# Optimization experiments

Hardware: AMD Instinct MI355X
Metric: run time of the kernel (lower is better)

## Reference

```python
import jax, jax.numpy as jnp
import numpy as np

ALPHA = 0.01  # alpha = input_scale * weight_scale (dequant scale)
BETA = 1.0    # bias scale, fixed to 1.0 in forward


def setup_inputs() -> dict:
    key = jax.random.key(0)
    k1, k2, k3 = jax.random.split(key, 3)
    # int8 values carried in int32 containers (schema has no int8 dtype)
    x = jax.random.randint(k1, (2, 2048, 4096), -127, 128, dtype=jnp.int32)
    weight = jax.random.randint(k2, (11008, 4096), -127, 128, dtype=jnp.int32)
    bias = jax.random.normal(k3, (1, 11008), dtype=jnp.float32)
    return {"x": x, "weight": weight, "bias": bias}


def reference(x, weight, bias):
    # x: [..., K] int8 activations, weight: [N, K] int8, bias: [1, N] fp32
    x_shape = x.shape
    x2 = x.reshape(-1, x_shape[-1]).astype(jnp.int8)   # [M, K]
    w8 = weight.astype(jnp.int8)                        # [N, K]
    acc = jnp.einsum('mk,nk->mn', x2, w8, preferred_element_type=jnp.int32)
    # fused dequant scale + fp32 bias add
    y = ALPHA * acc.astype(jnp.float32) + BETA * bias   # [M, N]
    return y.reshape(*x_shape[:-1], -1)
```

## Files before the change

kernel.cpp:

```cpp
#include <hip/hip_runtime.h>


#define M_DIM 4096
#define N_DIM 11008
#define K_DIM 4096
#define BM 256
#define BN 256
#define BK 128
#define NT (K_DIM / BK)
#define ALPHA 0.01f

typedef __attribute__((ext_vector_type(4))) int i32x4;

static __device__ __forceinline__ int pack4(int4 v) {
    return (v.x & 0xff) | ((v.y & 0xff) << 8) |
           ((v.z & 0xff) << 16) | ((unsigned)(v.w & 0xff) << 24);
}

__global__ __launch_bounds__(256) void pack_i8_kernel(
    const int4* __restrict__ x, int4* __restrict__ xout, int n16x,
    const int4* __restrict__ w, int4* __restrict__ wout, int n16_total)
{
    int i = blockIdx.x * blockDim.x + threadIdx.x;
    if (i >= n16_total) return;
    const int4* src;
    int4* dst;
    int idx;
    if (i < n16x) { src = x; dst = xout; idx = i; }
    else          { src = w; dst = wout; idx = i - n16x; }
    const int4* p = src + (size_t)4 * idx;
    int4 a = p[0], b = p[1], c = p[2], d = p[3];
    int4 r;
    r.x = pack4(a); r.y = pack4(b); r.z = pack4(c); r.w = pack4(d);
    dst[idx] = r;
}

#define GA0 (s_ + 8 * (s_ >> 3))
#define GA1 (8 + s_ + 8 * (s_ >> 3))

#define STAGE(dstArr, srcB, T, GEXPR)                                          \
    _Pragma("unroll") for (int u_ = 0; u_ < 2; u_++) {                         \
        const int s_ = u_ * 8 + wave;                                          \
        const int G_ = (GEXPR);                                                \
        __builtin_amdgcn_global_load_lds(                                      \
            (const __attribute__((address_space(1))) void*)(                   \
                (srcB) + (size_t)(G_ * 8 + (lane >> 3)) * K_DIM +              \
                (size_t)(T) * BK + sch16),                                     \
            (__attribute__((address_space(3))) void*)((dstArr) + G_ * 1024 +   \
                                                      lane * 16),              \
            16, 0, 0);                                                         \
    }

#define READ_A(Arr, dst, IB)                                                   \
    _Pragma("unroll") for (int i_ = 0; i_ < 4; i_++)                           \
        _Pragma("unroll") for (int k_ = 0; k_ < 2; k_++)                       \
            dst[i_][k_] = *(const i32x4*)((Arr) + aoff[k_] + ((IB) + i_) * 2048);

#define BLOAD01(dst, IMM)                                                      \
    _Pragma("unroll") for (int j_ = 0; j_ < 2; j_++)                           \
        _Pragma("unroll") for (int k_ = 0; k_ < 2; k_++)                       \
            dst[j_][k_] = *(const i32x4*)(bptr[j_] + (IMM) + k_ * 64);
#define BLOAD23(dst, IMM)                                                      \
    _Pragma("unroll") for (int j_ = 0; j_ < 2; j_++)                           \
        _Pragma("unroll") for (int k_ = 0; k_ < 2; k_++)                       \
            dst[j_][k_] = *(const i32x4*)(bptr[2 + j_] + (IMM) + k_ * 64);

#define MFMA_G(af, bf, IB, JB)                                                 \
    __builtin_amdgcn_s_setprio(1);                                             \
    _Pragma("unroll") for (int k_ = 0; k_ < 2; k_++)                           \
        _Pragma("unroll") for (int i_ = 0; i_ < 4; i_++)                       \
            _Pragma("unroll") for (int j_ = 0; j_ < 2; j_++)                   \
                acc[(IB) + i_][(JB) + j_] =                                    \
                    __builtin_amdgcn_mfma_i32_16x16x64_i8(                     \
                        af[i_][k_], bf[j_][k_],                                \
                        acc[(IB) + i_][(JB) + j_], 0, 0, 0);                   \
    __builtin_amdgcn_s_setprio(0);

#define VMCNT_(N) asm volatile("s_waitcnt vmcnt(" #N ")" ::: "memory")
#define VMCNT(N) VMCNT_(N)
#define BAR() __builtin_amdgcn_s_barrier()
#define SCHEDB() __builtin_amdgcn_sched_barrier(0)

#define TILE(CA, NA, B01c, B01n, T, KOFF, STG, V2, V4)                         \
    {                                                                          \
        READ_A(CA, ra, 0);                                             \
        if (STG) { STAGE(NA, Abase, (T) + 1, GA0); }                           \
        MFMA_G(ra, B01c, 0, 0);                                  \
        MFMA_G(ra, rb23, 0, 2);                                  \
        if (STG) { BLOAD01(B01n, (KOFF) + 128);                                \
                   STAGE(NA, Abase, (T) + 1, GA1); }                           \
        VMCNT(V2);                                                             \
        SCHEDB();                                                              \
        BAR();                                                    \
        READ_A(CA, ra, 4);                                             \
        MFMA_G(ra, rb23, 4, 2);                                  \
        if (STG) { BLOAD23(rb23, (KOFF) + 128); }                              \
        MFMA_G(ra, B01c, 4, 0);                                  \
        VMCNT(V4);                                                             \
        SCHEDB();                                                              \
        BAR();                                                    \
    }

__global__ __launch_bounds__(512, 1) void gemm_i8_kernel(
    const char* __restrict__ A,
    const char* __restrict__ B,
    const float* __restrict__ bias,
    float* __restrict__ C)
{
    __shared__ __attribute__((aligned(16))) char As0[BM * BK];
    __shared__ __attribute__((aligned(16))) char As1[BM * BK];

    const int tid   = threadIdx.x;
    const int lane  = tid & 63;
    const int wave  = tid >> 6;
    const int waveM = (wave >> 2) * 128;
    const int waveN = (wave & 3) * 64;
    const int lrow  = lane & 15;
    const int lquad = lane >> 4;

    const int bid = blockIdx.x;
    const int xcd = bid & 7;
    const int loc = bid >> 3;
    const int bm  = (2 * xcd + (loc & 1)) * BM;
    const int bn  = (loc >> 1) * BN;

    const int sch16 = ((lane & 7) ^ ((lane >> 3) & 7)) << 4;
    const char* Abase = A + (size_t)bm * K_DIM;

    int aoff[2];
#pragma unroll
    for (int ks = 0; ks < 2; ks++) {
        const int pos = ((ks * 4 + lquad) ^ (lrow & 7)) << 4;
        aoff[ks] = (waveM + lrow) * BK + pos;
    }

    const char* bptr[4];
#pragma unroll
    for (int j = 0; j < 4; j++)
        bptr[j] = B + (size_t)(bn + waveN + j * 16 + lrow) * K_DIM + lquad * 16;

    i32x4 acc[8][4] = {};
    i32x4 ra[4][2], rbA[2][2], rbB[2][2], rb23[2][2];

    STAGE(As0, Abase, 0, GA0);
    STAGE(As0, Abase, 0, GA1);
    BLOAD01(rbA, 0);
    BLOAD23(rb23, 0);
    VMCNT(0);
    BAR();

#pragma unroll 1
    for (int t = 0; t < NT - 4; t += 2) {
        TILE(As0, As1, rbA, rbB, t,     0,   1, 12, 10);
        TILE(As1, As0, rbB, rbA, t + 1, 128, 1, 12, 10);
#pragma unroll
        for (int j = 0; j < 4; j++) bptr[j] += 256;
    }
    TILE(As0, As1, rbA, rbB, NT - 4, 0,   1, 12, 10);
    TILE(As1, As0, rbB, rbA, NT - 3, 128, 1, 12, 10);
    TILE(As0, As1, rbA, rbB, NT - 2, 256, 1, 12, 10);
    TILE(As1, As0, rbB, rbA, NT - 1, 384, 0, 4, 0);

#pragma unroll
    for (int i = 0; i < 8; i++) {
        const int r0 = bm + waveM + i * 16 + lquad * 4;
#pragma unroll
        for (int j = 0; j < 4; j++) {
            const int c0 = bn + waveN + j * 16 + lrow;
            const float bv = bias[c0];
#pragma unroll
            for (int r = 0; r < 4; r++) {
                C[(size_t)(r0 + r) * N_DIM + c0] = ALPHA * (float)acc[i][j][r] + bv;
            }
        }
    }
}

extern "C" void kernel_launch(void* const* d_in, const int* in_sizes, int n_in,
                              void* d_out, int out_size, void* d_ws, size_t ws_size,
                              hipStream_t stream) {
    const int*   x    = (const int*)d_in[0];
    const int*   w    = (const int*)d_in[1];
    const float* bias = (const float*)d_in[2];
    float*       out  = (float*)d_out;

    char* Ap = (char*)d_ws;
    char* Wp = (char*)d_ws + (size_t)M_DIM * K_DIM;

    const int n16x = M_DIM * K_DIM / 16;
    const int n16w = N_DIM * K_DIM / 16;
    const int n16  = n16x + n16w;
    pack_i8_kernel<<<n16 / 256, 256, 0, stream>>>(
        (const int4*)x, (int4*)Ap, n16x, (const int4*)w, (int4*)Wp, n16);

    gemm_i8_kernel<<<dim3((M_DIM / BM) * (N_DIM / BN)), 512, 0, stream>>>(
        Ap, Wp, bias, out);
}
```

Measured before the change: 604.8 us.

## Pre-tile weights into 16x64 blocks and restructure the pipeline to one barrier per tile

The pack kernel now writes the int8 weight matrix as contiguous 1 KB blocks, each holding 16 rows by 64 k-bytes, laid out k-block-major. With that layout each wave's B-fragment loads become contiguous 1 KB reads through two running pointers, instead of strided row reads 4 KB apart. The main loop is also reordered: each tile waits on vmcnt and a single barrier, then issues all next-tile A staging and B loads up front. It uses two A register sets to overlap LDS reads with MFMAs. The cost is scattered 16-byte writes in the pack kernel and higher register pressure from the extra A fragments.

```diff
diff --git a/kernel.cpp b/kernel.cpp
--- a/kernel.cpp
+++ b/kernel.cpp
@@ -8,6 +8,8 @@
 #define BN 256
 #define BK 128
 #define NT (K_DIM / BK)
+#define NBLK (N_DIM / 16)
+#define KPBLK ((size_t)NBLK * 1024)
 #define ALPHA 0.01f
 
 typedef __attribute__((ext_vector_type(4))) int i32x4;
@@ -19,32 +21,40 @@
 
 __global__ __launch_bounds__(256) void pack_i8_kernel(
     const int4* __restrict__ x, int4* __restrict__ xout, int n16x,
-    const int4* __restrict__ w, int4* __restrict__ wout, int n16_total)
+    const int4* __restrict__ w, char* __restrict__ wout, int n16_total)
 {
     int i = blockIdx.x * blockDim.x + threadIdx.x;
     if (i >= n16_total) return;
-    const int4* src;
-    int4* dst;
-    int idx;
-    if (i < n16x) { src = x; dst = xout; idx = i; }
-    else          { src = w; dst = wout; idx = i - n16x; }
-    const int4* p = src + (size_t)4 * idx;
-    int4 a = p[0], b = p[1], c = p[2], d = p[3];
-    int4 r;
-    r.x = pack4(a); r.y = pack4(b); r.z = pack4(c); r.w = pack4(d);
-    dst[idx] = r;
+    if (i < n16x) {
+        const int4* p = x + (size_t)4 * i;
+        int4 a = p[0], b = p[1], c = p[2], d = p[3];
+        int4 r;
+        r.x = pack4(a); r.y = pack4(b); r.z = pack4(c); r.w = pack4(d);
+        xout[i] = r;
+    } else {
+        const int g = i - n16x;
+        const int4* p = w + (size_t)4 * g;
+        int4 a = p[0], b = p[1], c = p[2], d = p[3];
+        int4 r;
+        r.x = pack4(a); r.y = pack4(b); r.z = pack4(c); r.w = pack4(d);
+        const int n  = g >> 8;
+        const int k0 = (g & 255) << 4;
+        const size_t off = ((size_t)(k0 >> 6) * NBLK + (n >> 4)) * 1024
+                         + (size_t)((n & 15) << 6) + (k0 & 63);
+        *(int4*)(wout + off) = r;
+    }
 }
 
 #define GA0 (s_ + 8 * (s_ >> 3))
 #define GA1 (8 + s_ + 8 * (s_ >> 3))
 
-#define STAGE(dstArr, srcB, T, GEXPR)                                          \
+#define STAGE(dstArr, T, GEXPR)                                                \
     _Pragma("unroll") for (int u_ = 0; u_ < 2; u_++) {                         \
         const int s_ = u_ * 8 + wave;                                          \
         const int G_ = (GEXPR);                                                \
         __builtin_amdgcn_global_load_lds(                                      \
             (const __attribute__((address_space(1))) void*)(                   \
-                (srcB) + (size_t)(G_ * 8 + (lane >> 3)) * K_DIM +              \
+                Abase + (size_t)(G_ * 8 + (lane >> 3)) * K_DIM +               \
                 (size_t)(T) * BK + sch16),                                     \
             (__attribute__((address_space(3))) void*)((dstArr) + G_ * 1024 +   \
                                                       lane * 16),              \
@@ -56,14 +66,16 @@
         _Pragma("unroll") for (int k_ = 0; k_ < 2; k_++)                       \
             dst[i_][k_] = *(const i32x4*)((Arr) + aoff[k_] + ((IB) + i_) * 2048);
 
-#define BLOAD01(dst, IMM)                                                      \
-    _Pragma("unroll") for (int j_ = 0; j_ < 2; j_++)                           \
-        _Pragma("unroll") for (int k_ = 0; k_ < 2; k_++)                       \
-            dst[j_][k_] = *(const i32x4*)(bptr[j_] + (IMM) + k_ * 64);
-#define BLOAD23(dst, IMM)                                                      \
-    _Pragma("unroll") for (int j_ = 0; j_ < 2; j_++)                           \
-        _Pragma("unroll") for (int k_ = 0; k_ < 2; k_++)                       \
-            dst[j_][k_] = *(const i32x4*)(bptr[2 + j_] + (IMM) + k_ * 64);
+#define BLOAD01(dst)                                                           \
+    _Pragma("unroll") for (int j_ = 0; j_ < 2; j_++) {                         \
+        dst[j_][0] = *(const i32x4*)(bp0 + j_ * 1024);                         \
+        dst[j_][1] = *(const i32x4*)(bp1 + j_ * 1024);                         \
+    }
+#define BLOAD23(dst)                                                           \
+    _Pragma("unroll") for (int j_ = 0; j_ < 2; j_++) {                         \
+        dst[j_][0] = *(const i32x4*)(bp0 + 2048 + j_ * 1024);                  \
+        dst[j_][1] = *(const i32x4*)(bp1 + 2048 + j_ * 1024);                  \
+    }
 
 #define MFMA_G(af, bf, IB, JB)                                                 \
     __builtin_amdgcn_s_setprio(1);                                             \
@@ -81,24 +93,23 @@
 #define BAR() __builtin_amdgcn_s_barrier()
 #define SCHEDB() __builtin_amdgcn_sched_barrier(0)
 
-#define TILE(CA, NA, B01c, B01n, T, KOFF, STG, V2, V4)                         \
+#define TILE(CUR, NXT, B01c, B01n, T, STG)                                     \
     {                                                                          \
-        READ_A(CA, ra, 0);                                             \
-        if (STG) { STAGE(NA, Abase, (T) + 1, GA0); }                           \
-        MFMA_G(ra, B01c, 0, 0);                                  \
-        MFMA_G(ra, rb23, 0, 2);                                  \
-        if (STG) { BLOAD01(B01n, (KOFF) + 128);                                \
-                   STAGE(NA, Abase, (T) + 1, GA1); }                           \
-        VMCNT(V2);                                                             \
+        VMCNT(8);                                                              \
         SCHEDB();                                                              \
-        BAR();                                                    \
-        READ_A(CA, ra, 4);                                             \
-        MFMA_G(ra, rb23, 4, 2);                                  \
-        if (STG) { BLOAD23(rb23, (KOFF) + 128); }                              \
-        MFMA_G(ra, B01c, 4, 0);                                  \
-        VMCNT(V4);                                                             \
-        SCHEDB();                                                              \
-        BAR();                                                    \
+        BAR();                                                                 \
+        if (STG) {                                                             \
+            STAGE(NXT, (T) + 1, GA0);                                          \
+            STAGE(NXT, (T) + 1, GA1);                                          \
+            BLOAD01(B01n);                                                     \
+        }                                                                      \
+        READ_A(CUR, ra0, 0);                                                   \
+        MFMA_G(ra0, B01c, 0, 0);                                 \
+        MFMA_G(ra0, rb23, 0, 2);                                 \
+        READ_A(CUR, ra1, 4);                                                   \
+        MFMA_G(ra1, rb23, 4, 2);                                 \
+        if (STG) { BLOAD23(rb23); bp0 += 2 * KPBLK; bp1 += 2 * KPBLK; }        \
+        MFMA_G(ra1, B01c, 4, 0);                                 \
     }
 
 __global__ __launch_bounds__(512, 1) void gemm_i8_kernel(
@@ -134,32 +145,27 @@
         aoff[ks] = (waveM + lrow) * BK + pos;
     }
 
-    const char* bptr[4];
-#pragma unroll
-    for (int j = 0; j < 4; j++)
-        bptr[j] = B + (size_t)(bn + waveN + j * 16 + lrow) * K_DIM + lquad * 16;
+    const char* bp0 = B + ((size_t)((bn + waveN) >> 4)) * 1024
+                    + (size_t)(((lane & 15) << 6) + ((lane >> 4) << 4));
+    const char* bp1 = bp0 + KPBLK;
 
     i32x4 acc[8][4] = {};
-    i32x4 ra[4][2], rbA[2][2], rbB[2][2], rb23[2][2];
-
-    STAGE(As0, Abase, 0, GA0);
-    STAGE(As0, Abase, 0, GA1);
-    BLOAD01(rbA, 0);
-    BLOAD23(rb23, 0);
-    VMCNT(0);
-    BAR();
+    i32x4 ra0[4][2], ra1[4][2], rbA[2][2], rbB[2][2], rb23[2][2];
+
+    STAGE(As0, 0, GA0);
+    STAGE(As0, 0, GA1);
+    BLOAD01(rbA);
+    BLOAD23(rb23);
+    bp0 += 2 * KPBLK;
+    bp1 += 2 * KPBLK;
 
 #pragma unroll 1
-    for (int t = 0; t < NT - 4; t += 2) {
-        TILE(As0, As1, rbA, rbB, t,     0,   1, 12, 10);
-        TILE(As1, As0, rbB, rbA, t + 1, 128, 1, 12, 10);
-#pragma unroll
-        for (int j = 0; j < 4; j++) bptr[j] += 256;
-    }
-    TILE(As0, As1, rbA, rbB, NT - 4, 0,   1, 12, 10);
-    TILE(As1, As0, rbB, rbA, NT - 3, 128, 1, 12, 10);
-    TILE(As0, As1, rbA, rbB, NT - 2, 256, 1, 12, 10);
-    TILE(As1, As0, rbB, rbA, NT - 1, 384, 0, 4, 0);
+    for (int t = 0; t < NT - 2; t += 2) {
+        TILE(As0, As1, rbA, rbB, t,     1);
+        TILE(As1, As0, rbB, rbA, t + 1, 1);
+    }
+    TILE(As0, As1, rbA, rbB, NT - 2, 1);
+    TILE(As1, As0, rbB, rbA, NT - 1, 0);
 
 #pragma unroll
     for (int i = 0; i < 8; i++) {
@@ -191,7 +197,7 @@
     const int n16w = N_DIM * K_DIM / 16;
     const int n16  = n16x + n16w;
     pack_i8_kernel<<<n16 / 256, 256, 0, stream>>>(
-        (const int4*)x, (int4*)Ap, n16x, (const int4*)w, (int4*)Wp, n16);
+        (const int4*)x, (int4*)Ap, n16x, (const int4*)w, Wp, n16);
 
     gemm_i8_kernel<<<dim3((M_DIM / BM) * (N_DIM / BN)), 512, 0, stream>>>(
         Ap, Wp, bias, out);
```

After: 533.9 us. 11.7% less time.
